# Kernel optimization log

Hardware: AMD Instinct MI355X
Metric: run time of the kernel (lower is better)

The kernel has to match this reference:

```python
import jax, jax.numpy as jnp
import numpy as np

HEADS = 8
HEIGHT = 512
WIDTH = 512
LATENT = 64  # height // 8
N_INST = 8


def setup_inputs() -> dict:
    key = jax.random.key(0)
    ks = jax.random.split(key, 8)
    C, Cx, L, N = 320, 768, 77, N_INST
    HW = LATENT * LATENT
    hidden_states = jax.random.normal(ks[0], (2, HW, C), jnp.float32)
    encoder_hidden_states = jax.random.normal(ks[1], (N + 3, L, Cx), jnp.float32)
    # non-degenerate normalized boxes (x0, y0, x1, y1)
    rng = np.random.default_rng(0)
    x0 = rng.uniform(0.0, 0.5, (N,)).astype(np.float32)
    y0 = rng.uniform(0.0, 0.5, (N,)).astype(np.float32)
    x1 = (x0 + rng.uniform(0.2, 0.45, (N,))).astype(np.float32)
    y1 = (y0 + rng.uniform(0.2, 0.45, (N,))).astype(np.float32)
    bboxes = jnp.asarray(np.stack([x0, y0, x1, y1], axis=-1)[None], jnp.float32)  # (1, N, 4)
    s = 0.02
    Wq = jax.random.normal(ks[2], (C, C), jnp.float32) * s
    Wk = jax.random.normal(ks[3], (Cx, C), jnp.float32) * s
    Wv = jax.random.normal(ks[4], (Cx, C), jnp.float32) * s
    Wo = jax.random.normal(ks[5], (C, C), jnp.float32) * s
    bo = jnp.zeros((C,), jnp.float32)
    return dict(hidden_states=hidden_states, encoder_hidden_states=encoder_hidden_states,
                bboxes=bboxes, Wq=Wq, Wk=Wk, Wv=Wv, Wo=Wo, bo=bo)


def _heads(x):
    # (B, S, H*D) -> (B*H, S, D)   [diffusers head_to_batch_dim]
    B, S, C = x.shape
    D = C // HEADS
    return x.reshape(B, S, HEADS, D).transpose(0, 2, 1, 3).reshape(B * HEADS, S, D)


def _unheads(x):
    # (B*H, S, D) -> (B, S, H*D)   [diffusers batch_to_head_dim]
    BH, S, D = x.shape
    B = BH // HEADS
    return x.reshape(B, HEADS, S, D).transpose(0, 2, 1, 3).reshape(B, S, HEADS * D)


def _forward(hidden_states, encoder_hidden_states, bboxes, Wq, Wk, Wv, Wo, bo):
    N = bboxes.shape[1]
    HW = hidden_states.shape[1]
    # drop the extra (MIGC) text embedding row, as in the processor
    ehs = encoder_hidden_states[:-1]  # (N+2, L, Cx)
    # batch = [uncond, cond repeated instance_num+1 times]
    hs = jnp.concatenate([hidden_states[:1],
                          jnp.repeat(hidden_states[1:2], N + 1, axis=0)], axis=0)  # (N+2, HW, C)
    q = _heads(hs @ Wq)
    k = _heads(ehs @ Wk)
    v = _heads(ehs @ Wv)
    scale = 1.0 / jnp.sqrt(jnp.asarray(q.shape[-1], q.dtype))
    probs = jax.nn.softmax(jnp.einsum('bqd,bkd->bqk', q, k) * scale, axis=-1)  # ((N+2)*H, HW, L)
    out = _unheads(jnp.einsum('bqk,bkd->bqd', probs, v))  # (N+2, HW, C)
    out = out @ Wo + bo
    hs_uncond = out[:1]
    cond_ca = out[1:][None]  # (1, N+1, HW, C)
    # rasterize per-instance bbox masks at full res (int() truncation == floor for positives)
    b = bboxes[0]  # (N, 4) = x0, y0, x1, y1
    w_min = jnp.floor(WIDTH * b[:, 0])[:, None, None]
    w_max = jnp.floor(WIDTH * b[:, 2])[:, None, None]
    h_min = jnp.floor(HEIGHT * b[:, 1])[:, None, None]
    h_max = jnp.floor(HEIGHT * b[:, 3])[:, None, None]
    rows = jnp.arange(HEIGHT, dtype=jnp.float32)[None, :, None]
    cols = jnp.arange(WIDTH, dtype=jnp.float32)[None, None, :]
    masks = ((rows >= h_min) & (rows < h_max) & (cols >= w_min) & (cols < w_max)).astype(jnp.float32)  # (N,H,W)
    gmask = jax.image.resize(masks, (N, LATENT, LATENT), method='bilinear')  # (N, 64, 64)
    # NaiveFuser: phase weights = [0.1 (full prompt), 10*mask_i], normalized sum over phases
    phase_w = jnp.concatenate([jnp.full((1, HW), 0.1, jnp.float32),
                               gmask.reshape(N, HW) * 10.0], axis=0)  # (N+1, HW)
    w = phase_w[None, :, :, None]  # (1, N+1, HW, 1)
    fused = (cond_ca * w).sum(axis=1) / (w.sum(axis=1) + 1e-6)  # (1, HW, C)
    return jnp.concatenate([hs_uncond, fused], axis=0)  # (2, HW, C)


def reference(hidden_states, encoder_hidden_states, bboxes, Wq, Wk, Wv, Wo, bo):
    return _forward(hidden_states, encoder_hidden_states, bboxes, Wq, Wk, Wv, Wo, bo)
```

## Files before the change

kernel.cpp:

```cpp
#include <hip/hip_runtime.h>
#include <math.h>

#define HW 4096
#define C 320
#define CX 768
#define L 77
#define NB 10
#define NH 8
#define HD 40
#define NINST 8
#define KVC 640
#define SCALE 0.15811388300841898f
#define PSTR 104
#define KSTR 48
#define VSTR 104

typedef _Float16 half8v __attribute__((ext_vector_type(8)));
typedef _Float16 half4v __attribute__((ext_vector_type(4)));
typedef float f32x4 __attribute__((ext_vector_type(4)));

#define KBH (80 * KSTR)
#define VBH (48 * VSTR)

#define SEG_MASK   16
#define N_CVT1     (2 * HW * C / 4)
#define N_CVT2     (NB * L * CX / 4)
#define SEG_CVT    (((N_CVT1 + N_CVT2) + 255) / 256)
#define SEG_WPACK  240
#define SEG_VTZ    195
#define SEG_KPAD   6
#define NPREP      (SEG_MASK + SEG_CVT + SEG_WPACK + SEG_VTZ + SEG_KPAD)

__device__ __forceinline__ float axis_profile(int o, float lo, float hi) {
    float num = 0.f, den = 0.f;
    int j0 = 8 * o - 4;
#pragma unroll
    for (int t = 0; t < 16; ++t) {
        int j = j0 + t;
        float wt = 1.0f - fabsf((float)t - 7.5f) * 0.125f;
        if (j >= 0 && j < 512) {
            den += wt;
            float fj = (float)j;
            if (fj >= lo && fj < hi) num += wt;
        }
    }
    return num / den;
}

__global__ __launch_bounds__(256) void prep_kernel(
        const float* __restrict__ bboxes,
        const float* __restrict__ hs, const float* __restrict__ ehs,
        const float* __restrict__ Wq, const float* __restrict__ Wk,
        const float* __restrict__ Wv, const float* __restrict__ Wo,
        float* __restrict__ wPh, float* __restrict__ wSum,
        _Float16* __restrict__ hsH, _Float16* __restrict__ ehsH,
        _Float16* __restrict__ WqT, _Float16* __restrict__ WkvT,
        _Float16* __restrict__ WoT, _Float16* __restrict__ VTg,
        _Float16* __restrict__ Khp) {
    __shared__ float tile[64][65];
    __shared__ float sw_s[NINST][64];
    __shared__ float sh_s[NINST][4];
    int bx = blockIdx.x, tid = threadIdx.x;

    if (bx < SEG_MASK) {
        int oyb = bx * 4;
        for (int i = tid; i < NINST * 64; i += 256) {
            int n = i >> 6, ox = i & 63;
            float lo = floorf(512.f * bboxes[n * 4 + 0]);
            float hi = floorf(512.f * bboxes[n * 4 + 2]);
            sw_s[n][ox] = axis_profile(ox, lo, hi);
        }
        if (tid < NINST * 4) {
            int n = tid >> 2, oy = tid & 3;
            float lo = floorf(512.f * bboxes[n * 4 + 1]);
            float hi = floorf(512.f * bboxes[n * 4 + 3]);
            sh_s[n][oy] = axis_profile(oyb + oy, lo, hi);
        }
        __syncthreads();
        int oy = tid >> 6, ox = tid & 63;
        int hw = (oyb + oy) * 64 + ox;
        float sum = 0.1f;
        wPh[hw] = 0.1f;
#pragma unroll
        for (int n = 0; n < NINST; ++n) {
            float wv = 10.f * sh_s[n][oy] * sw_s[n][ox];
            wPh[(n + 1) * HW + hw] = wv;
            sum += wv;
        }
        wSum[hw] = sum;
    } else if (bx < SEG_MASK + SEG_CVT) {
        int i = (bx - SEG_MASK) * 256 + tid;
        const float* src; _Float16* dst;
        if (i < N_CVT1) { src = hs; dst = hsH; }
        else if (i < N_CVT1 + N_CVT2) { i -= N_CVT1; src = ehs; dst = ehsH; }
        else return;
        float4 v = ((const float4*)src)[i];
        half4v h = {(_Float16)v.x, (_Float16)v.y, (_Float16)v.z, (_Float16)v.w};
        ((half4v*)dst)[i] = h;
    } else if (bx < SEG_MASK + SEG_CVT + SEG_WPACK) {
        int zz = bx - SEG_MASK - SEG_CVT;
        int z = zz / 60, inner = zz - z * 60;
        int by = inner / 5, bx2 = inner - by * 5;
        const float* W; _Float16* WT; int K;
        if (z == 0)      { W = Wq; WT = WqT; K = C; }
        else if (z == 1) { W = Wk; WT = WkvT; K = CX; }
        else if (z == 2) { W = Wv; WT = WkvT + (size_t)C * CX; K = CX; }
        else             { W = Wo; WT = WoT; K = C; }
        int kt = by * 64;
        if (kt >= K) return;
        int nt = bx2 * 64;
#pragma unroll
        for (int p = 0; p < 16; ++p) {
            int idx = p * 256 + tid;
            int k = idx >> 6, n = idx & 63;
            tile[k][n] = W[(size_t)(kt + k) * C + nt + n];
        }
        __syncthreads();
#pragma unroll
        for (int p = 0; p < 16; ++p) {
            int idx = p * 256 + tid;
            int n = idx >> 6, k = idx & 63;
            WT[(size_t)(nt + n) * K + kt + k] = (_Float16)tile[k][n];
        }
    } else if (bx < SEG_MASK + SEG_CVT + SEG_WPACK + SEG_VTZ) {
        int i = (bx - SEG_MASK - SEG_CVT - SEG_WPACK) * 256 + tid;
        int e0 = i * 8;
        int rem = e0 % VBH;
        int d = rem / VSTR;
        int key0 = rem % VSTR;
        half8v v;
#pragma unroll
        for (int j = 0; j < 8; ++j)
            v[j] = (_Float16)((d == 40 && (key0 + j) < 77) ? 1.f : 0.f);
        ((half8v*)VTg)[i] = v;
    } else {
        int i = (bx - SEG_MASK - SEG_CVT - SEG_WPACK - SEG_VTZ) * 256 + tid;
        if (i < 1440) {
            int rowIdx = i / 6, c8 = i - rowIdx * 6;
            int bh = rowIdx / 3;
            int key = 77 + rowIdx - bh * 3;
            half8v z8 = {(_Float16)0.f,(_Float16)0.f,(_Float16)0.f,(_Float16)0.f,
                         (_Float16)0.f,(_Float16)0.f,(_Float16)0.f,(_Float16)0.f};
            *(half8v*)(Khp + ((size_t)bh * 80 + key) * KSTR + c8 * 8) = z8;
        }
    }
}

__global__ __launch_bounds__(256) void gemm_kv(const _Float16* __restrict__ A,
                                               const _Float16* __restrict__ BT,
                                               _Float16* __restrict__ Khp,
                                               _Float16* __restrict__ VTg) {
    const int K = CX, M = NB * L;
    int lane = threadIdx.x & 63, wave = threadIdx.x >> 6;
    int m0 = blockIdx.y * 64 + wave * 16;
    int n0 = blockIdx.x * 64;
    int lr = lane & 15, kq = (lane >> 4) * 8;
    int arow = m0 + lr; if (arow >= M) arow = M - 1;
    const _Float16* ap = A + (size_t)arow * K + kq;
    const _Float16* bp = BT + (size_t)(n0 + lr) * K + kq;
    f32x4 acc0 = {0.f,0.f,0.f,0.f}, acc1 = acc0, acc2 = acc0, acc3 = acc0;
    for (int k0 = 0; k0 < K; k0 += 32) {
        half8v af = *(const half8v*)(ap + k0);
        half8v b0 = *(const half8v*)(bp + k0);
        half8v b1 = *(const half8v*)(bp + (size_t)16 * K + k0);
        half8v b2 = *(const half8v*)(bp + (size_t)32 * K + k0);
        half8v b3 = *(const half8v*)(bp + (size_t)48 * K + k0);
        acc0 = __builtin_amdgcn_mfma_f32_16x16x32_f16(af, b0, acc0, 0, 0, 0);
        acc1 = __builtin_amdgcn_mfma_f32_16x16x32_f16(af, b1, acc1, 0, 0, 0);
        acc2 = __builtin_amdgcn_mfma_f32_16x16x32_f16(af, b2, acc2, 0, 0, 0);
        acc3 = __builtin_amdgcn_mfma_f32_16x16x32_f16(af, b3, acc3, 0, 0, 0);
    }
    int rb = m0 + ((lane >> 4) << 2);
    f32x4 accs[4] = {acc0, acc1, acc2, acc3};
#pragma unroll
    for (int t = 0; t < 4; ++t) {
        int col = n0 + t * 16 + lr;
#pragma unroll
        for (int r = 0; r < 4; ++r) {
            int row = rb + r;
            if (row < M) {
                int bb = row / 77;
                int key = row - bb * 77;
                if (col < C) {
                    int h = col / HD, d = col - h * HD;
                    Khp[((size_t)(bb * 8 + h) * 80 + key) * KSTR + d] = (_Float16)accs[t][r];
                } else {
                    int ch = col - C;
                    int h = ch / HD, d = ch - h * HD;
                    VTg[((size_t)(bb * 8 + h) * 48 + d) * VSTR + key] = (_Float16)accs[t][r];
                }
            }
        }
    }
}

__global__ __launch_bounds__(256, 2) void attn_mfma(const _Float16* __restrict__ hsH,
                                                    const _Float16* __restrict__ WqT,
                                                    const _Float16* __restrict__ Khp,
                                                    const _Float16* __restrict__ VTg,
                                                    const float* __restrict__ wPh,
                                                    _Float16* __restrict__ Xh) {
    __shared__ _Float16 smem[2 * (KBH + VBH) + 4 * 2 * 16 * PSTR];
    _Float16* Ks0 = smem;
    _Float16* Vs0 = smem + KBH;
    _Float16* Ks1 = smem + KBH + VBH;
    _Float16* Vs1 = smem + 2 * KBH + VBH;
    _Float16* pbase = smem + 2 * (KBH + VBH);

    int tid = threadIdx.x;
    int wave = tid >> 6, lane = tid & 63;
    int head = blockIdx.x >> 6;
    int qg = blockIdx.x & 63;
    int qrow0 = qg * 64 + wave * 16;
    int c = lane & 15, quad = lane >> 4;
    _Float16* pl0 = pbase + (size_t)(wave * 2) * 16 * PSTR;
    _Float16* pl1 = pl0 + 16 * PSTR;
    half8v zero8 = {(_Float16)0.f,(_Float16)0.f,(_Float16)0.f,(_Float16)0.f,
                    (_Float16)0.f,(_Float16)0.f,(_Float16)0.f,(_Float16)0.f};

    const half8v* Kg8 = (const half8v*)(Khp + (size_t)head * KBH);
    const half8v* Vg8 = (const half8v*)(VTg + (size_t)head * VBH);
    const size_t kstep = (size_t)8 * KBH / 8;
    const size_t vstep = (size_t)8 * VBH / 8;

    half8v kr0, kr1, vr0, vr1, vr2;
    kr0 = Kg8[tid];
    if (tid < 224) kr1 = Kg8[tid + 256];
    vr0 = Vg8[tid];
    vr1 = Vg8[tid + 256];
    if (tid < 112) vr2 = Vg8[tid + 512];

#pragma unroll
    for (int i = 0; i < 4; ++i) {
        int idx = i * 64 + lane;
        if (idx < 224) {
            int buf = idx / 112;
            int rem = idx - buf * 112;
            int row = rem / 7, ch = rem - row * 7;
            _Float16* pb = buf ? pl1 : pl0;
            *(half8v*)&pb[row * PSTR + 40 + ch * 8] = zero8;
        }
    }

    {
        const _Float16* bu = hsH + (size_t)(qrow0 + c) * C + quad * 8;
        const _Float16* bc = bu + (size_t)HW * C;
        f32x4 qa0[3] = {}, qa1[3] = {};
        for (int k0 = 0; k0 < C; k0 += 32) {
            half8v hu = *(const half8v*)(bu + k0);
            half8v hc = *(const half8v*)(bc + k0);
#pragma unroll
            for (int t = 0; t < 3; ++t) {
                const _Float16* ap = WqT + (size_t)(head * HD + t * 16 + c) * C + quad * 8 + k0;
                half8v af = *(const half8v*)ap;
                qa0[t] = __builtin_amdgcn_mfma_f32_16x16x32_f16(af, hu, qa0[t], 0, 0, 0);
                qa1[t] = __builtin_amdgcn_mfma_f32_16x16x32_f16(af, hc, qa1[t], 0, 0, 0);
            }
        }
#pragma unroll
        for (int t = 0; t < 3; ++t) {
            if (t < 2 || quad < 2) {
                half4v h0 = {(_Float16)(qa0[t][0] * SCALE), (_Float16)(qa0[t][1] * SCALE),
                             (_Float16)(qa0[t][2] * SCALE), (_Float16)(qa0[t][3] * SCALE)};
                half4v h1 = {(_Float16)(qa1[t][0] * SCALE), (_Float16)(qa1[t][1] * SCALE),
                             (_Float16)(qa1[t][2] * SCALE), (_Float16)(qa1[t][3] * SCALE)};
                *(half4v*)(pl0 + c * PSTR + t * 16 + quad * 4) = h0;
                *(half4v*)(pl1 + c * PSTR + t * 16 + quad * 4) = h1;
            }
        }
    }
    half8v qu0 = *(const half8v*)(pl0 + (size_t)c * PSTR + quad * 8);
    half8v qu1 = *(const half8v*)(pl0 + (size_t)c * PSTR + 32 + quad * 8);
    half8v qc0 = *(const half8v*)(pl1 + (size_t)c * PSTR + quad * 8);
    half8v qc1 = *(const half8v*)(pl1 + (size_t)c * PSTR + 32 + quad * 8);

    {
        half8v* Kd = (half8v*)Ks0;
        half8v* Vd = (half8v*)Vs0;
        Kd[tid] = kr0;
        if (tid < 224) Kd[tid + 256] = kr1;
        Vd[tid] = vr0;
        Vd[tid + 256] = vr1;
        if (tid < 112) Vd[tid + 512] = vr2;
    }
    __syncthreads();

    f32x4 oacc[3] = {};
    int srcl = 32 + c;

    for (int b = 0; b < NB; ++b) {
        if (b + 1 < NB) {
            const half8v* Kn = Kg8 + (size_t)(b + 1) * 8 * (KBH / 8);
            const half8v* Vn = Vg8 + (size_t)(b + 1) * 8 * (VBH / 8);
            kr0 = Kn[tid];
            if (tid < 224) kr1 = Kn[tid + 256];
            vr0 = Vn[tid];
            vr1 = Vn[tid + 256];
            if (tid < 112) vr2 = Vn[tid + 512];
        }

        _Float16* Kb = (b & 1) ? Ks1 : Ks0;
        _Float16* Vb = (b & 1) ? Vs1 : Vs0;
        half8v qb0 = b ? qc0 : qu0;
        half8v qb1 = b ? qc1 : qu1;
        float w = b ? wPh[(size_t)(b - 1) * HW + qrow0 + c] : 1.f;

        f32x4 s[5];
#pragma unroll
        for (int u = 0; u < 5; ++u) {
            half8v ka0 = *(const half8v*)&Kb[(u * 16 + c) * KSTR + quad * 8];
            half8v ka1 = *(const half8v*)&Kb[(u * 16 + c) * KSTR + 32 + quad * 8];
            f32x4 a = {0.f,0.f,0.f,0.f};
            a = __builtin_amdgcn_mfma_f32_16x16x32_f16(ka0, qb0, a, 0, 0, 0);
            a = __builtin_amdgcn_mfma_f32_16x16x32_f16(ka1, qb1, a, 0, 0, 0);
            s[u] = a;
        }

#pragma unroll
        for (int u = 0; u < 5; ++u) {
            half4v h = {(_Float16)__expf(s[u][0]), (_Float16)__expf(s[u][1]),
                        (_Float16)__expf(s[u][2]), (_Float16)__expf(s[u][3])};
            *(half4v*)(pl0 + c * PSTR + u * 16 + quad * 4) = h;
        }
        half8v p0 = *(const half8v*)(pl0 + (size_t)c * PSTR + quad * 8);
        half8v p1 = *(const half8v*)(pl0 + (size_t)c * PSTR + 32 + quad * 8);
        half8v p2 = *(const half8v*)(pl0 + (size_t)c * PSTR + 64 + quad * 8);

        f32x4 ox[3];
#pragma unroll
        for (int t = 0; t < 3; ++t) {
            half8v va0 = *(const half8v*)&Vb[(t * 16 + c) * VSTR + quad * 8];
            half8v va1 = *(const half8v*)&Vb[(t * 16 + c) * VSTR + 32 + quad * 8];
            half8v va2 = *(const half8v*)&Vb[(t * 16 + c) * VSTR + 64 + quad * 8];
            f32x4 a = {0.f,0.f,0.f,0.f};
            a = __builtin_amdgcn_mfma_f32_16x16x32_f16(va0, p0, a, 0, 0, 0);
            a = __builtin_amdgcn_mfma_f32_16x16x32_f16(va1, p1, a, 0, 0, 0);
            a = __builtin_amdgcn_mfma_f32_16x16x32_f16(va2, p2, a, 0, 0, 0);
            ox[t] = a;
        }

        float l = __shfl(ox[2][0], srcl, 64);

        if (b == 0) {
            float rin = 1.0f / l;
#pragma unroll
            for (int t = 0; t < 3; ++t) {
                if (t < 2 || quad < 2) {
                    half4v h = {(_Float16)(ox[t][0] * rin), (_Float16)(ox[t][1] * rin),
                                (_Float16)(ox[t][2] * rin), (_Float16)(ox[t][3] * rin)};
                    *(half4v*)(Xh + (size_t)(qrow0 + c) * C + head * HD + t * 16 + quad * 4) = h;
                }
            }
        } else {
            float rf = w / l;
#pragma unroll
            for (int t = 0; t < 3; ++t) {
                oacc[t][0] += ox[t][0] * rf;
                oacc[t][1] += ox[t][1] * rf;
                oacc[t][2] += ox[t][2] * rf;
                oacc[t][3] += ox[t][3] * rf;
            }
        }

        if (b + 1 < NB) {
            half8v* Kd = (half8v*)((b & 1) ? Ks0 : Ks1);
            half8v* Vd = (half8v*)((b & 1) ? Vs0 : Vs1);
            Kd[tid] = kr0;
            if (tid < 224) Kd[tid + 256] = kr1;
            Vd[tid] = vr0;
            Vd[tid + 256] = vr1;
            if (tid < 112) Vd[tid + 512] = vr2;
        }
        __syncthreads();
    }

#pragma unroll
    for (int t = 0; t < 3; ++t) {
        if (t < 2 || quad < 2) {
            half4v h = {(_Float16)oacc[t][0], (_Float16)oacc[t][1],
                        (_Float16)oacc[t][2], (_Float16)oacc[t][3]};
            *(half4v*)(Xh + (size_t)(HW + qrow0 + c) * C + head * HD + t * 16 + quad * 4) = h;
        }
    }
}

__global__ __launch_bounds__(256) void gemm_oproj_f16(const _Float16* __restrict__ A,
                                                      const _Float16* __restrict__ BT,
                                                      const float* __restrict__ bo,
                                                      const float* __restrict__ wSum,
                                                      float* __restrict__ Out) {
    const int K = C;
    __shared__ _Float16 Bs[64 * 328];
    int tid = threadIdx.x;
    int n0 = blockIdx.x * 64;
    for (int i = tid; i < 64 * 40; i += 256) {
        int row = i / 40, c8 = i - row * 40;
        *(half8v*)&Bs[row * 328 + c8 * 8] =
            *(const half8v*)(BT + (size_t)(n0 + row) * K + c8 * 8);
    }
    __syncthreads();

    int lane = tid & 63, wave = tid >> 6;
    int m0 = blockIdx.y * 64 + wave * 16;
    int lr = lane & 15, kq = (lane >> 4) * 8;
    const _Float16* ap = A + (size_t)(m0 + lr) * K + kq;
    f32x4 acc0 = {0.f,0.f,0.f,0.f}, acc1 = acc0, acc2 = acc0, acc3 = acc0;
#pragma unroll
    for (int k0 = 0; k0 < K; k0 += 32) {
        half8v af = *(const half8v*)(ap + k0);
        half8v b0 = *(const half8v*)&Bs[(0 * 16 + lr) * 328 + k0 + kq];
        half8v b1 = *(const half8v*)&Bs[(1 * 16 + lr) * 328 + k0 + kq];
        half8v b2 = *(const half8v*)&Bs[(2 * 16 + lr) * 328 + k0 + kq];
        half8v b3 = *(const half8v*)&Bs[(3 * 16 + lr) * 328 + k0 + kq];
        acc0 = __builtin_amdgcn_mfma_f32_16x16x32_f16(af, b0, acc0, 0, 0, 0);
        acc1 = __builtin_amdgcn_mfma_f32_16x16x32_f16(af, b1, acc1, 0, 0, 0);
        acc2 = __builtin_amdgcn_mfma_f32_16x16x32_f16(af, b2, acc2, 0, 0, 0);
        acc3 = __builtin_amdgcn_mfma_f32_16x16x32_f16(af, b3, acc3, 0, 0, 0);
    }
    int rb = m0 + ((lane >> 4) << 2);
    f32x4 accs[4] = {acc0, acc1, acc2, acc3};
#pragma unroll
    for (int t = 0; t < 4; ++t) {
        int col = n0 + t * 16 + lr;
        float bv = bo[col];
#pragma unroll
        for (int r = 0; r < 4; ++r) {
            int row = rb + r;
            float v = accs[t][r];
            if (row < HW) {
                v += bv;
            } else {
                float ws = wSum[row - HW];
                v = (v + bv * ws) / (ws + 1e-6f);
            }
            Out[(size_t)row * C + col] = v;
        }
    }
}

extern "C" void kernel_launch(void* const* d_in, const int* in_sizes, int n_in,
                              void* d_out, int out_size, void* d_ws, size_t ws_size,
                              hipStream_t stream) {
    const float* hs   = (const float*)d_in[0];
    const float* ehs  = (const float*)d_in[1];
    const float* bbox = (const float*)d_in[2];
    const float* Wq   = (const float*)d_in[3];
    const float* Wk   = (const float*)d_in[4];
    const float* Wv   = (const float*)d_in[5];
    const float* Wo   = (const float*)d_in[6];
    const float* bo   = (const float*)d_in[7];
    float* out = (float*)d_out;

    float* wPh  = (float*)d_ws;
    float* wSum = wPh + (size_t)9 * HW;
    _Float16* hsH  = (_Float16*)(wSum + HW);
    _Float16* ehsH = hsH + (size_t)2 * HW * C;
    _Float16* WqT  = ehsH + (size_t)NB * L * CX;
    _Float16* WkvT = WqT + (size_t)C * C;
    _Float16* WoT  = WkvT + (size_t)KVC * CX;
    _Float16* Khp  = WoT + (size_t)C * C;
    _Float16* VTg  = Khp + (size_t)80 * KBH;
    _Float16* Xh   = VTg + (size_t)80 * VBH;

    prep_kernel<<<dim3(NPREP), 256, 0, stream>>>(bbox, hs, ehs, Wq, Wk, Wv, Wo,
                                                 wPh, wSum, hsH, ehsH, WqT, WkvT, WoT,
                                                 VTg, Khp);
    gemm_kv<<<dim3(KVC / 64, (NB * L + 63) / 64), 256, 0, stream>>>(ehsH, WkvT, Khp, VTg);
    attn_mfma<<<dim3(NH * 64), 256, 0, stream>>>(hsH, WqT, Khp, VTg, wPh, Xh);
    gemm_oproj_f16<<<dim3(C / 64, (2 * HW) / 64), 256, 0, stream>>>(Xh, WoT, bo, wSum, out);
}
```

Baseline: 132.8 us.

## Fuse four kernel launches into one cooperative persistent kernel with grid syncs

Replaces the prep, KV-GEMM, attention and output-projection launches with a single cooperative kernel that loops over work units per stage and separates stages with grid.sync(). The goal is to remove three kernel-launch gaps and their tail effects. In exchange, the grid is capped at 512 blocks (or the occupancy limit), and some stages such as prep (over 600 units) and oproj (640 units) must loop. Grid-wide barriers also add their own cost. A fallback to the original four launches is kept in case the cooperative launch fails.

Result: slower. 264.6 us (+99.3%).

```diff
diff --git a/kernel.cpp b/kernel.cpp
--- a/kernel.cpp
+++ b/kernel.cpp
@@ -1,5 +1,8 @@
 #include <hip/hip_runtime.h>
+#include <hip/hip_cooperative_groups.h>
 #include <math.h>
+
+namespace cg = cooperative_groups;
 
 #define HW 4096
 #define C 320
@@ -31,6 +34,11 @@
 #define SEG_KPAD   6
 #define NPREP      (SEG_MASK + SEG_CVT + SEG_WPACK + SEG_VTZ + SEG_KPAD)
 
+#define KV_UNITS    130
+#define ATTN_UNITS  (NH * 64)
+#define OPROJ_UNITS 640
+#define SMEM_BYTES  61952
+
 __device__ __forceinline__ float axis_profile(int o, float lo, float hi) {
     float num = 0.f, den = 0.f;
     int j0 = 8 * o - 4;
@@ -45,6 +53,398 @@
         }
     }
     return num / den;
+}
+
+__global__ __launch_bounds__(256, 2) void fused_kernel(
+        const float* __restrict__ bboxes, const float* __restrict__ hs,
+        const float* __restrict__ ehs, const float* __restrict__ Wq,
+        const float* __restrict__ Wk, const float* __restrict__ Wv,
+        const float* __restrict__ Wo, const float* __restrict__ bo,
+        float* __restrict__ wPh, float* __restrict__ wSum,
+        _Float16* __restrict__ hsH, _Float16* __restrict__ ehsH,
+        _Float16* __restrict__ WqT, _Float16* __restrict__ WkvT,
+        _Float16* __restrict__ WoT, _Float16* __restrict__ Khp,
+        _Float16* __restrict__ VTg, _Float16* __restrict__ Xh,
+        float* __restrict__ Out) {
+    cg::grid_group grid = cg::this_grid();
+    __shared__ __align__(16) unsigned char smem_raw[SMEM_BYTES];
+    const int tid = threadIdx.x;
+    const int gsz = gridDim.x;
+
+    {
+        float (*tile)[65] = (float (*)[65])smem_raw;
+        float (*sw_s)[64] = (float (*)[64])(smem_raw + 64 * 65 * 4);
+        float (*sh_s)[4]  = (float (*)[4])(smem_raw + 64 * 65 * 4 + NINST * 64 * 4);
+        for (int s = blockIdx.x; s < NPREP; s += gsz) {
+            if (s < SEG_MASK) {
+                int oyb = s * 4;
+                for (int i = tid; i < NINST * 64; i += 256) {
+                    int n = i >> 6, ox = i & 63;
+                    float lo = floorf(512.f * bboxes[n * 4 + 0]);
+                    float hi = floorf(512.f * bboxes[n * 4 + 2]);
+                    sw_s[n][ox] = axis_profile(ox, lo, hi);
+                }
+                if (tid < NINST * 4) {
+                    int n = tid >> 2, oy = tid & 3;
+                    float lo = floorf(512.f * bboxes[n * 4 + 1]);
+                    float hi = floorf(512.f * bboxes[n * 4 + 3]);
+                    sh_s[n][oy] = axis_profile(oyb + oy, lo, hi);
+                }
+                __syncthreads();
+                int oy = tid >> 6, ox = tid & 63;
+                int hw = (oyb + oy) * 64 + ox;
+                float sum = 0.1f;
+                wPh[hw] = 0.1f;
+#pragma unroll
+                for (int n = 0; n < NINST; ++n) {
+                    float wv = 10.f * sh_s[n][oy] * sw_s[n][ox];
+                    wPh[(n + 1) * HW + hw] = wv;
+                    sum += wv;
+                }
+                wSum[hw] = sum;
+            } else if (s < SEG_MASK + SEG_CVT) {
+                int i = (s - SEG_MASK) * 256 + tid;
+                if (i < N_CVT1) {
+                    float4 v = ((const float4*)hs)[i];
+                    half4v h = {(_Float16)v.x, (_Float16)v.y, (_Float16)v.z, (_Float16)v.w};
+                    ((half4v*)hsH)[i] = h;
+                } else if (i < N_CVT1 + N_CVT2) {
+                    int j = i - N_CVT1;
+                    float4 v = ((const float4*)ehs)[j];
+                    half4v h = {(_Float16)v.x, (_Float16)v.y, (_Float16)v.z, (_Float16)v.w};
+                    ((half4v*)ehsH)[j] = h;
+                }
+            } else if (s < SEG_MASK + SEG_CVT + SEG_WPACK) {
+                int zz = s - SEG_MASK - SEG_CVT;
+                int z = zz / 60, inner = zz - z * 60;
+                int by = inner / 5, bx2 = inner - by * 5;
+                const float* W; _Float16* WT; int K;
+                if (z == 0)      { W = Wq; WT = WqT; K = C; }
+                else if (z == 1) { W = Wk; WT = WkvT; K = CX; }
+                else if (z == 2) { W = Wv; WT = WkvT + (size_t)C * CX; K = CX; }
+                else             { W = Wo; WT = WoT; K = C; }
+                int kt = by * 64;
+                if (kt < K) {
+                    int nt = bx2 * 64;
+#pragma unroll
+                    for (int p = 0; p < 16; ++p) {
+                        int idx = p * 256 + tid;
+                        int k = idx >> 6, n = idx & 63;
+                        tile[k][n] = W[(size_t)(kt + k) * C + nt + n];
+                    }
+                    __syncthreads();
+#pragma unroll
+                    for (int p = 0; p < 16; ++p) {
+                        int idx = p * 256 + tid;
+                        int n = idx >> 6, k = idx & 63;
+                        WT[(size_t)(nt + n) * K + kt + k] = (_Float16)tile[k][n];
+                    }
+                }
+            } else if (s < SEG_MASK + SEG_CVT + SEG_WPACK + SEG_VTZ) {
+                int i = (s - SEG_MASK - SEG_CVT - SEG_WPACK) * 256 + tid;
+                int e0 = i * 8;
+                int rem = e0 % VBH;
+                int d = rem / VSTR;
+                int key0 = rem % VSTR;
+                half8v v;
+#pragma unroll
+                for (int j = 0; j < 8; ++j)
+                    v[j] = (_Float16)((d == 40 && (key0 + j) < 77) ? 1.f : 0.f);
+                ((half8v*)VTg)[i] = v;
+            } else {
+                int i = (s - SEG_MASK - SEG_CVT - SEG_WPACK - SEG_VTZ) * 256 + tid;
+                if (i < 1440) {
+                    int rowIdx = i / 6, c8 = i - rowIdx * 6;
+                    int bh = rowIdx / 3;
+                    int key = 77 + rowIdx - bh * 3;
+                    half8v z8 = {(_Float16)0.f,(_Float16)0.f,(_Float16)0.f,(_Float16)0.f,
+                                 (_Float16)0.f,(_Float16)0.f,(_Float16)0.f,(_Float16)0.f};
+                    *(half8v*)(Khp + ((size_t)bh * 80 + key) * KSTR + c8 * 8) = z8;
+                }
+            }
+            __syncthreads();
+        }
+    }
+    grid.sync();
+
+    for (int u = blockIdx.x; u < KV_UNITS; u += gsz) {
+        const int K = CX, M = NB * L;
+        int lane = tid & 63, wave = tid >> 6;
+        int m0 = (u / 10) * 64 + wave * 16;
+        int n0 = (u % 10) * 64;
+        int lr = lane & 15, kq = (lane >> 4) * 8;
+        int arow = m0 + lr; if (arow >= M) arow = M - 1;
+        const _Float16* ap = ehsH + (size_t)arow * K + kq;
+        const _Float16* bp = WkvT + (size_t)(n0 + lr) * K + kq;
+        f32x4 acc0 = {0.f,0.f,0.f,0.f}, acc1 = acc0, acc2 = acc0, acc3 = acc0;
+        for (int k0 = 0; k0 < K; k0 += 32) {
+            half8v af = *(const half8v*)(ap + k0);
+            half8v b0 = *(const half8v*)(bp + k0);
+            half8v b1 = *(const half8v*)(bp + (size_t)16 * K + k0);
+            half8v b2 = *(const half8v*)(bp + (size_t)32 * K + k0);
+            half8v b3 = *(const half8v*)(bp + (size_t)48 * K + k0);
+            acc0 = __builtin_amdgcn_mfma_f32_16x16x32_f16(af, b0, acc0, 0, 0, 0);
+            acc1 = __builtin_amdgcn_mfma_f32_16x16x32_f16(af, b1, acc1, 0, 0, 0);
+            acc2 = __builtin_amdgcn_mfma_f32_16x16x32_f16(af, b2, acc2, 0, 0, 0);
+            acc3 = __builtin_amdgcn_mfma_f32_16x16x32_f16(af, b3, acc3, 0, 0, 0);
+        }
+        int rb = m0 + ((lane >> 4) << 2);
+        f32x4 accs[4] = {acc0, acc1, acc2, acc3};
+#pragma unroll
+        for (int t = 0; t < 4; ++t) {
+            int col = n0 + t * 16 + lr;
+#pragma unroll
+            for (int r = 0; r < 4; ++r) {
+                int row = rb + r;
+                if (row < M) {
+                    int bb = row / 77;
+                    int key = row - bb * 77;
+                    if (col < C) {
+                        int h = col / HD, d = col - h * HD;
+                        Khp[((size_t)(bb * 8 + h) * 80 + key) * KSTR + d] = (_Float16)accs[t][r];
+                    } else {
+                        int ch = col - C;
+                        int h = ch / HD, d = ch - h * HD;
+                        VTg[((size_t)(bb * 8 + h) * 48 + d) * VSTR + key] = (_Float16)accs[t][r];
+                    }
+                }
+            }
+        }
+    }
+    grid.sync();
+
+    for (int u = blockIdx.x; u < ATTN_UNITS; u += gsz) {
+        _Float16* smemH = (_Float16*)smem_raw;
+        _Float16* Ks0 = smemH;
+        _Float16* Vs0 = smemH + KBH;
+        _Float16* Ks1 = smemH + KBH + VBH;
+        _Float16* Vs1 = smemH + 2 * KBH + VBH;
+        _Float16* pbase = smemH + 2 * (KBH + VBH);
+
+        int wave = tid >> 6, lane = tid & 63;
+        int head = u >> 6;
+        int qg = u & 63;
+        int qrow0 = qg * 64 + wave * 16;
+        int c = lane & 15, quad = lane >> 4;
+        _Float16* pl0 = pbase + (size_t)(wave * 2) * 16 * PSTR;
+        _Float16* pl1 = pl0 + 16 * PSTR;
+        half8v zero8 = {(_Float16)0.f,(_Float16)0.f,(_Float16)0.f,(_Float16)0.f,
+                        (_Float16)0.f,(_Float16)0.f,(_Float16)0.f,(_Float16)0.f};
+
+        const half8v* Kg8 = (const half8v*)(Khp + (size_t)head * KBH);
+        const half8v* Vg8 = (const half8v*)(VTg + (size_t)head * VBH);
+
+        half8v kr0, kr1, vr0, vr1, vr2;
+        kr0 = Kg8[tid];
+        if (tid < 224) kr1 = Kg8[tid + 256];
+        vr0 = Vg8[tid];
+        vr1 = Vg8[tid + 256];
+        if (tid < 112) vr2 = Vg8[tid + 512];
+
+#pragma unroll
+        for (int i = 0; i < 4; ++i) {
+            int idx = i * 64 + lane;
+            if (idx < 224) {
+                int buf = idx / 112;
+                int rem = idx - buf * 112;
+                int row = rem / 7, ch = rem - row * 7;
+                _Float16* pb = buf ? pl1 : pl0;
+                *(half8v*)&pb[row * PSTR + 40 + ch * 8] = zero8;
+            }
+        }
+
+        {
+            const _Float16* bu = hsH + (size_t)(qrow0 + c) * C + quad * 8;
+            const _Float16* bc = bu + (size_t)HW * C;
+            f32x4 qa0[3] = {}, qa1[3] = {};
+            for (int k0 = 0; k0 < C; k0 += 32) {
+                half8v hu = *(const half8v*)(bu + k0);
+                half8v hc = *(const half8v*)(bc + k0);
+#pragma unroll
+                for (int t = 0; t < 3; ++t) {
+                    const _Float16* ap = WqT + (size_t)(head * HD + t * 16 + c) * C + quad * 8 + k0;
+                    half8v af = *(const half8v*)ap;
+                    qa0[t] = __builtin_amdgcn_mfma_f32_16x16x32_f16(af, hu, qa0[t], 0, 0, 0);
+                    qa1[t] = __builtin_amdgcn_mfma_f32_16x16x32_f16(af, hc, qa1[t], 0, 0, 0);
+                }
+            }
+#pragma unroll
+            for (int t = 0; t < 3; ++t) {
+                if (t < 2 || quad < 2) {
+                    half4v h0 = {(_Float16)(qa0[t][0] * SCALE), (_Float16)(qa0[t][1] * SCALE),
+                                 (_Float16)(qa0[t][2] * SCALE), (_Float16)(qa0[t][3] * SCALE)};
+                    half4v h1 = {(_Float16)(qa1[t][0] * SCALE), (_Float16)(qa1[t][1] * SCALE),
+                                 (_Float16)(qa1[t][2] * SCALE), (_Float16)(qa1[t][3] * SCALE)};
+                    *(half4v*)(pl0 + c * PSTR + t * 16 + quad * 4) = h0;
+                    *(half4v*)(pl1 + c * PSTR + t * 16 + quad * 4) = h1;
+                }
+            }
+        }
+        half8v qu0 = *(const half8v*)(pl0 + (size_t)c * PSTR + quad * 8);
+        half8v qu1 = *(const half8v*)(pl0 + (size_t)c * PSTR + 32 + quad * 8);
+        half8v qc0 = *(const half8v*)(pl1 + (size_t)c * PSTR + quad * 8);
+        half8v qc1 = *(const half8v*)(pl1 + (size_t)c * PSTR + 32 + quad * 8);
+
+        {
+            half8v* Kd = (half8v*)Ks0;
+            half8v* Vd = (half8v*)Vs0;
+            Kd[tid] = kr0;
+            if (tid < 224) Kd[tid + 256] = kr1;
+            Vd[tid] = vr0;
+            Vd[tid + 256] = vr1;
+            if (tid < 112) Vd[tid + 512] = vr2;
+        }
+        __syncthreads();
+
+        f32x4 oacc[3] = {};
+        int srcl = 32 + c;
+
+        for (int b = 0; b < NB; ++b) {
+            if (b + 1 < NB) {
+                const half8v* Kn = Kg8 + (size_t)(b + 1) * 8 * (KBH / 8);
+                const half8v* Vn = Vg8 + (size_t)(b + 1) * 8 * (VBH / 8);
+                kr0 = Kn[tid];
+                if (tid < 224) kr1 = Kn[tid + 256];
+                vr0 = Vn[tid];
+                vr1 = Vn[tid + 256];
+                if (tid < 112) vr2 = Vn[tid + 512];
+            }
+
+            _Float16* Kb = (b & 1) ? Ks1 : Ks0;
+            _Float16* Vb = (b & 1) ? Vs1 : Vs0;
+            half8v qb0 = b ? qc0 : qu0;
+            half8v qb1 = b ? qc1 : qu1;
+            float w = b ? wPh[(size_t)(b - 1) * HW + qrow0 + c] : 1.f;
+
+            f32x4 s[5];
+#pragma unroll
+            for (int v = 0; v < 5; ++v) {
+                half8v ka0 = *(const half8v*)&Kb[(v * 16 + c) * KSTR + quad * 8];
+                half8v ka1 = *(const half8v*)&Kb[(v * 16 + c) * KSTR + 32 + quad * 8];
+                f32x4 a = {0.f,0.f,0.f,0.f};
+                a = __builtin_amdgcn_mfma_f32_16x16x32_f16(ka0, qb0, a, 0, 0, 0);
+                a = __builtin_amdgcn_mfma_f32_16x16x32_f16(ka1, qb1, a, 0, 0, 0);
+                s[v] = a;
+            }
+
+#pragma unroll
+            for (int v = 0; v < 5; ++v) {
+                half4v h = {(_Float16)__expf(s[v][0]), (_Float16)__expf(s[v][1]),
+                            (_Float16)__expf(s[v][2]), (_Float16)__expf(s[v][3])};
+                *(half4v*)(pl0 + c * PSTR + v * 16 + quad * 4) = h;
+            }
+            half8v p0 = *(const half8v*)(pl0 + (size_t)c * PSTR + quad * 8);
+            half8v p1 = *(const half8v*)(pl0 + (size_t)c * PSTR + 32 + quad * 8);
+            half8v p2 = *(const half8v*)(pl0 + (size_t)c * PSTR + 64 + quad * 8);
+
+            f32x4 ox[3];
+#pragma unroll
+            for (int t = 0; t < 3; ++t) {
+                half8v va0 = *(const half8v*)&Vb[(t * 16 + c) * VSTR + quad * 8];
+                half8v va1 = *(const half8v*)&Vb[(t * 16 + c) * VSTR + 32 + quad * 8];
+                half8v va2 = *(const half8v*)&Vb[(t * 16 + c) * VSTR + 64 + quad * 8];
+                f32x4 a = {0.f,0.f,0.f,0.f};
+                a = __builtin_amdgcn_mfma_f32_16x16x32_f16(va0, p0, a, 0, 0, 0);
+                a = __builtin_amdgcn_mfma_f32_16x16x32_f16(va1, p1, a, 0, 0, 0);
+                a = __builtin_amdgcn_mfma_f32_16x16x32_f16(va2, p2, a, 0, 0, 0);
+                ox[t] = a;
+            }
+
+            float l = __shfl(ox[2][0], srcl, 64);
+
+            if (b == 0) {
+                float rin = 1.0f / l;
+#pragma unroll
+                for (int t = 0; t < 3; ++t) {
+                    if (t < 2 || quad < 2) {
+                        half4v h = {(_Float16)(ox[t][0] * rin), (_Float16)(ox[t][1] * rin),
+                                    (_Float16)(ox[t][2] * rin), (_Float16)(ox[t][3] * rin)};
+                        *(half4v*)(Xh + (size_t)(qrow0 + c) * C + head * HD + t * 16 + quad * 4) = h;
+                    }
+                }
+            } else {
+                float rf = w / l;
+#pragma unroll
+                for (int t = 0; t < 3; ++t) {
+                    oacc[t][0] += ox[t][0] * rf;
+                    oacc[t][1] += ox[t][1] * rf;
+                    oacc[t][2] += ox[t][2] * rf;
+                    oacc[t][3] += ox[t][3] * rf;
+                }
+            }
+
+            if (b + 1 < NB) {
+                half8v* Kd = (half8v*)((b & 1) ? Ks0 : Ks1);
+                half8v* Vd = (half8v*)((b & 1) ? Vs0 : Vs1);
+                Kd[tid] = kr0;
+                if (tid < 224) Kd[tid + 256] = kr1;
+                Vd[tid] = vr0;
+                Vd[tid + 256] = vr1;
+                if (tid < 112) Vd[tid + 512] = vr2;
+            }
+            __syncthreads();
+        }
+
+#pragma unroll
+        for (int t = 0; t < 3; ++t) {
+            if (t < 2 || quad < 2) {
+                half4v h = {(_Float16)oacc[t][0], (_Float16)oacc[t][1],
+                            (_Float16)oacc[t][2], (_Float16)oacc[t][3]};
+                *(half4v*)(Xh + (size_t)(HW + qrow0 + c) * C + head * HD + t * 16 + quad * 4) = h;
+            }
+        }
+    }
+    grid.sync();
+
+    for (int u = blockIdx.x; u < OPROJ_UNITS; u += gsz) {
+        _Float16* Bs = (_Float16*)smem_raw;
+        const int K = C;
+        int n0 = (u % 5) * 64;
+        for (int i = tid; i < 64 * 40; i += 256) {
+            int row = i / 40, c8 = i - row * 40;
+            *(half8v*)&Bs[row * 328 + c8 * 8] =
+                *(const half8v*)(WoT + (size_t)(n0 + row) * K + c8 * 8);
+        }
+        __syncthreads();
+
+        int lane = tid & 63, wave = tid >> 6;
+        int m0 = (u / 5) * 64 + wave * 16;
+        int lr = lane & 15, kq = (lane >> 4) * 8;
+        const _Float16* ap = Xh + (size_t)(m0 + lr) * K + kq;
+        f32x4 acc0 = {0.f,0.f,0.f,0.f}, acc1 = acc0, acc2 = acc0, acc3 = acc0;
+#pragma unroll
+        for (int k0 = 0; k0 < K; k0 += 32) {
+            half8v af = *(const half8v*)(ap + k0);
+            half8v b0 = *(const half8v*)&Bs[(0 * 16 + lr) * 328 + k0 + kq];
+            half8v b1 = *(const half8v*)&Bs[(1 * 16 + lr) * 328 + k0 + kq];
+            half8v b2 = *(const half8v*)&Bs[(2 * 16 + lr) * 328 + k0 + kq];
+            half8v b3 = *(const half8v*)&Bs[(3 * 16 + lr) * 328 + k0 + kq];
+            acc0 = __builtin_amdgcn_mfma_f32_16x16x32_f16(af, b0, acc0, 0, 0, 0);
+            acc1 = __builtin_amdgcn_mfma_f32_16x16x32_f16(af, b1, acc1, 0, 0, 0);
+            acc2 = __builtin_amdgcn_mfma_f32_16x16x32_f16(af, b2, acc2, 0, 0, 0);
+            acc3 = __builtin_amdgcn_mfma_f32_16x16x32_f16(af, b3, acc3, 0, 0, 0);
+        }
+        int rb = m0 + ((lane >> 4) << 2);
+        f32x4 accs[4] = {acc0, acc1, acc2, acc3};
+#pragma unroll
+        for (int t = 0; t < 4; ++t) {
+            int col = n0 + t * 16 + lr;
+            float bv = bo[col];
+#pragma unroll
+            for (int r = 0; r < 4; ++r) {
+                int row = rb + r;
+                float v = accs[t][r];
+                if (row < HW) {
+                    v += bv;
+                } else {
+                    float ws = wSum[row - HW];
+                    v = (v + bv * ws) / (ws + 1e-6f);
+                }
+                Out[(size_t)row * C + col] = v;
+            }
+        }
+        __syncthreads();
+    }
 }
 
 __global__ __launch_bounds__(256) void prep_kernel(
@@ -220,8 +620,6 @@
 
     const half8v* Kg8 = (const half8v*)(Khp + (size_t)head * KBH);
     const half8v* Vg8 = (const half8v*)(VTg + (size_t)head * VBH);
-    const size_t kstep = (size_t)8 * KBH / 8;
-    const size_t vstep = (size_t)8 * VBH / 8;
 
     half8v kr0, kr1, vr0, vr1, vr2;
     kr0 = Kg8[tid];
@@ -462,10 +860,44 @@
     _Float16* VTg  = Khp + (size_t)80 * KBH;
     _Float16* Xh   = VTg + (size_t)80 * VBH;
 
-    prep_kernel<<<dim3(NPREP), 256, 0, stream>>>(bbox, hs, ehs, Wq, Wk, Wv, Wo,
-                                                 wPh, wSum, hsH, ehsH, WqT, WkvT, WoT,
-                                                 VTg, Khp);
-    gemm_kv<<<dim3(KVC / 64, (NB * L + 63) / 64), 256, 0, stream>>>(ehsH, WkvT, Khp, VTg);
-    attn_mfma<<<dim3(NH * 64), 256, 0, stream>>>(hsH, WqT, Khp, VTg, wPh, Xh);
-    gemm_oproj_f16<<<dim3(C / 64, (2 * HW) / 64), 256, 0, stream>>>(Xh, WoT, bo, wSum, out);
+    static int nblk = -1;
+    if (nblk < 0) {
+        int dev = 0;
+        (void)hipGetDevice(&dev);
+        int coop = 0;
+        (void)hipDeviceGetAttribute(&coop, hipDeviceAttributeCooperativeLaunch, dev);
+        if (!coop) {
+            nblk = 0;
+        } else {
+            int per_cu = 0;
+            if (hipOccupancyMaxActiveBlocksPerMultiprocessor(
+                    &per_cu, (const void*)fused_kernel, 256, 0) != hipSuccess || per_cu <= 0)
+                per_cu = 2;
+            int ncu = 256;
+            hipDeviceProp_t prop;
+            if (hipGetDeviceProperties(&prop, dev) == hipSuccess && prop.multiProcessorCount > 0)
+                ncu = prop.multiProcessorCount;
+            long cap = (long)per_cu * (long)ncu;
+            nblk = cap < ATTN_UNITS ? (int)cap : ATTN_UNITS;
+            if (nblk < 1) nblk = 1;
+        }
+    }
+
+    hipError_t err = hipErrorUnknown;
+    if (nblk > 0) {
+        void* args[] = {(void*)&bbox, (void*)&hs, (void*)&ehs, (void*)&Wq, (void*)&Wk,
+                        (void*)&Wv, (void*)&Wo, (void*)&bo, (void*)&wPh, (void*)&wSum,
+                        (void*)&hsH, (void*)&ehsH, (void*)&WqT, (void*)&WkvT, (void*)&WoT,
+                        (void*)&Khp, (void*)&VTg, (void*)&Xh, (void*)&out};
+        err = hipLaunchCooperativeKernel((const void*)fused_kernel, dim3(nblk), dim3(256),
+                                         args, 0, stream);
+    }
+    if (err != hipSuccess) {
+        prep_kernel<<<dim3(NPREP), 256, 0, stream>>>(bbox, hs, ehs, Wq, Wk, Wv, Wo,
+                                                     wPh, wSum, hsH, ehsH, WqT, WkvT, WoT,
+                                                     VTg, Khp);
+        gemm_kv<<<dim3(KVC / 64, (NB * L + 63) / 64), 256, 0, stream>>>(ehsH, WkvT, Khp, VTg);
+        attn_mfma<<<dim3(NH * 64), 256, 0, stream>>>(hsH, WqT, Khp, VTg, wPh, Xh);
+        gemm_oproj_f16<<<dim3(C / 64, (2 * HW) / 64), 256, 0, stream>>>(Xh, WoT, bo, wSum, out);
+    }
 }
```

## Fuse K/V projection GEMM into prep kernel reading fp32 inputs directly

Applied to the files above, without the earlier changes.

The separate gemm_kv launch is folded into the prep kernel as an extra block segment. That segment converts fp32 encoder states and Wk/Wv to fp16 on the fly, so the ehs conversion pass and the Wk/Wv transpose-pack pass are no longer needed. The V padding init is narrowed to write only the pad regions (rows 40-47 and keys 77-103), so it no longer overwrites the whole buffer and races with the fused GEMM writes. This drops one launch and several intermediate buffers. The cost is strided scalar fp32 weight loads in the GEMM inner loop, which are much less coalesced than the old packed fp16 loads.

Result: no change. 133.0 us (+0.1%).

```diff
diff --git a/kernel.cpp b/kernel.cpp
--- a/kernel.cpp
+++ b/kernel.cpp
@@ -22,14 +22,15 @@
 #define KBH (80 * KSTR)
 #define VBH (48 * VSTR)
 
+#define SEG_KV     130
 #define SEG_MASK   16
 #define N_CVT1     (2 * HW * C / 4)
-#define N_CVT2     (NB * L * CX / 4)
-#define SEG_CVT    (((N_CVT1 + N_CVT2) + 255) / 256)
-#define SEG_WPACK  240
-#define SEG_VTZ    195
+#define SEG_CVTH   (N_CVT1 / 256)
+#define SEG_WPK    50
+#define SEG_VT40   33
+#define SEG_VTP    338
 #define SEG_KPAD   6
-#define NPREP      (SEG_MASK + SEG_CVT + SEG_WPACK + SEG_VTZ + SEG_KPAD)
+#define NPREP (SEG_KV + SEG_MASK + SEG_CVTH + SEG_WPK + SEG_VT40 + SEG_VTP + SEG_KPAD)
 
 __device__ __forceinline__ float axis_profile(int o, float lo, float hi) {
     float num = 0.f, den = 0.f;
@@ -47,23 +48,80 @@
     return num / den;
 }
 
-__global__ __launch_bounds__(256) void prep_kernel(
+__global__ __launch_bounds__(256) void prep_kv_kernel(
         const float* __restrict__ bboxes,
         const float* __restrict__ hs, const float* __restrict__ ehs,
         const float* __restrict__ Wq, const float* __restrict__ Wk,
         const float* __restrict__ Wv, const float* __restrict__ Wo,
         float* __restrict__ wPh, float* __restrict__ wSum,
-        _Float16* __restrict__ hsH, _Float16* __restrict__ ehsH,
-        _Float16* __restrict__ WqT, _Float16* __restrict__ WkvT,
-        _Float16* __restrict__ WoT, _Float16* __restrict__ VTg,
-        _Float16* __restrict__ Khp) {
+        _Float16* __restrict__ hsH,
+        _Float16* __restrict__ WqT, _Float16* __restrict__ WoT,
+        _Float16* __restrict__ VTg, _Float16* __restrict__ Khp) {
     __shared__ float tile[64][65];
     __shared__ float sw_s[NINST][64];
     __shared__ float sh_s[NINST][4];
     int bx = blockIdx.x, tid = threadIdx.x;
 
-    if (bx < SEG_MASK) {
-        int oyb = bx * 4;
+    if (bx < SEG_KV) {
+        const int K = CX, M = NB * L;
+        int lane = tid & 63, wave = tid >> 6;
+        int m0 = (bx / 10) * 64 + wave * 16;
+        int n0 = (bx % 10) * 64;
+        int lr = lane & 15, kq = (lane >> 4) * 8;
+        int arow = m0 + lr; if (arow >= M) arow = M - 1;
+        const float* ap = ehs + (size_t)arow * K + kq;
+        const float* wp[4];
+        int cols[4];
+#pragma unroll
+        for (int t = 0; t < 4; ++t) {
+            int col = n0 + t * 16 + lr;
+            cols[t] = col;
+            wp[t] = (col < C) ? (Wk + col) : (Wv + (col - C));
+        }
+        f32x4 acc0 = {0.f,0.f,0.f,0.f}, acc1 = acc0, acc2 = acc0, acc3 = acc0;
+        for (int k0 = 0; k0 < K; k0 += 32) {
+            float4 a0 = *(const float4*)(ap + k0);
+            float4 a1 = *(const float4*)(ap + k0 + 4);
+            half8v af = {(_Float16)a0.x, (_Float16)a0.y, (_Float16)a0.z, (_Float16)a0.w,
+                         (_Float16)a1.x, (_Float16)a1.y, (_Float16)a1.z, (_Float16)a1.w};
+            half8v bf0, bf1, bf2, bf3;
+#pragma unroll
+            for (int j = 0; j < 8; ++j) {
+                size_t kk = (size_t)(k0 + kq + j) * C;
+                bf0[j] = (_Float16)wp[0][kk];
+                bf1[j] = (_Float16)wp[1][kk];
+                bf2[j] = (_Float16)wp[2][kk];
+                bf3[j] = (_Float16)wp[3][kk];
+            }
+            acc0 = __builtin_amdgcn_mfma_f32_16x16x32_f16(af, bf0, acc0, 0, 0, 0);
+            acc1 = __builtin_amdgcn_mfma_f32_16x16x32_f16(af, bf1, acc1, 0, 0, 0);
+            acc2 = __builtin_amdgcn_mfma_f32_16x16x32_f16(af, bf2, acc2, 0, 0, 0);
+            acc3 = __builtin_amdgcn_mfma_f32_16x16x32_f16(af, bf3, acc3, 0, 0, 0);
+        }
+        int rb = m0 + ((lane >> 4) << 2);
+        f32x4 accs[4] = {acc0, acc1, acc2, acc3};
+#pragma unroll
+        for (int t = 0; t < 4; ++t) {
+            int col = cols[t];
+#pragma unroll
+            for (int r = 0; r < 4; ++r) {
+                int row = rb + r;
+                if (row < M) {
+                    int bb = row / 77;
+                    int key = row - bb * 77;
+                    if (col < C) {
+                        int h = col / HD, d = col - h * HD;
+                        Khp[((size_t)(bb * 8 + h) * 80 + key) * KSTR + d] = (_Float16)accs[t][r];
+                    } else {
+                        int ch = col - C;
+                        int h = ch / HD, d = ch - h * HD;
+                        VTg[((size_t)(bb * 8 + h) * 48 + d) * VSTR + key] = (_Float16)accs[t][r];
+                    }
+                }
+            }
+        }
+    } else if (bx < SEG_KV + SEG_MASK) {
+        int oyb = (bx - SEG_KV) * 4;
         for (int i = tid; i < NINST * 64; i += 256) {
             int n = i >> 6, ox = i & 63;
             float lo = floorf(512.f * bboxes[n * 4 + 0]);
@@ -88,27 +146,18 @@
             sum += wv;
         }
         wSum[hw] = sum;
-    } else if (bx < SEG_MASK + SEG_CVT) {
-        int i = (bx - SEG_MASK) * 256 + tid;
-        const float* src; _Float16* dst;
-        if (i < N_CVT1) { src = hs; dst = hsH; }
-        else if (i < N_CVT1 + N_CVT2) { i -= N_CVT1; src = ehs; dst = ehsH; }
-        else return;
-        float4 v = ((const float4*)src)[i];
+    } else if (bx < SEG_KV + SEG_MASK + SEG_CVTH) {
+        int i = (bx - SEG_KV - SEG_MASK) * 256 + tid;
+        float4 v = ((const float4*)hs)[i];
         half4v h = {(_Float16)v.x, (_Float16)v.y, (_Float16)v.z, (_Float16)v.w};
-        ((half4v*)dst)[i] = h;
-    } else if (bx < SEG_MASK + SEG_CVT + SEG_WPACK) {
-        int zz = bx - SEG_MASK - SEG_CVT;
-        int z = zz / 60, inner = zz - z * 60;
+        ((half4v*)hsH)[i] = h;
+    } else if (bx < SEG_KV + SEG_MASK + SEG_CVTH + SEG_WPK) {
+        int zz = bx - SEG_KV - SEG_MASK - SEG_CVTH;
+        int z = zz / 25, inner = zz - z * 25;
         int by = inner / 5, bx2 = inner - by * 5;
-        const float* W; _Float16* WT; int K;
-        if (z == 0)      { W = Wq; WT = WqT; K = C; }
-        else if (z == 1) { W = Wk; WT = WkvT; K = CX; }
-        else if (z == 2) { W = Wv; WT = WkvT + (size_t)C * CX; K = CX; }
-        else             { W = Wo; WT = WoT; K = C; }
-        int kt = by * 64;
-        if (kt >= K) return;
-        int nt = bx2 * 64;
+        const float* W = z ? Wo : Wq;
+        _Float16* WT = z ? WoT : WqT;
+        int kt = by * 64, nt = bx2 * 64;
 #pragma unroll
         for (int p = 0; p < 16; ++p) {
             int idx = p * 256 + tid;
@@ -120,21 +169,29 @@
         for (int p = 0; p < 16; ++p) {
             int idx = p * 256 + tid;
             int n = idx >> 6, k = idx & 63;
-            WT[(size_t)(nt + n) * K + kt + k] = (_Float16)tile[k][n];
-        }
-    } else if (bx < SEG_MASK + SEG_CVT + SEG_WPACK + SEG_VTZ) {
-        int i = (bx - SEG_MASK - SEG_CVT - SEG_WPACK) * 256 + tid;
-        int e0 = i * 8;
-        int rem = e0 % VBH;
-        int d = rem / VSTR;
-        int key0 = rem % VSTR;
-        half8v v;
-#pragma unroll
-        for (int j = 0; j < 8; ++j)
-            v[j] = (_Float16)((d == 40 && (key0 + j) < 77) ? 1.f : 0.f);
-        ((half8v*)VTg)[i] = v;
+            WT[(size_t)(nt + n) * C + kt + k] = (_Float16)tile[k][n];
+        }
+    } else if (bx < SEG_KV + SEG_MASK + SEG_CVTH + SEG_WPK + SEG_VT40) {
+        int i = (bx - SEG_KV - SEG_MASK - SEG_CVTH - SEG_WPK) * 256 + tid;
+        if (i < 8320) {
+            int bh = i / 104, rem = i - bh * 104;
+            int d = 40 + rem / 13, c8 = rem - (rem / 13) * 13;
+            int key0 = c8 * 8;
+            half8v v;
+#pragma unroll
+            for (int j = 0; j < 8; ++j)
+                v[j] = (_Float16)((d == 40 && (key0 + j) < 77) ? 1.f : 0.f);
+            *(half8v*)(VTg + (size_t)bh * VBH + (size_t)d * VSTR + key0) = v;
+        }
+    } else if (bx < SEG_KV + SEG_MASK + SEG_CVTH + SEG_WPK + SEG_VT40 + SEG_VTP) {
+        int i = (bx - SEG_KV - SEG_MASK - SEG_CVTH - SEG_WPK - SEG_VT40) * 256 + tid;
+        if (i < 86400) {
+            int r = i / 27, kk = 77 + (i - r * 27);
+            int bh = r / 40, d = r - bh * 40;
+            VTg[(size_t)bh * VBH + (size_t)d * VSTR + kk] = (_Float16)0.f;
+        }
     } else {
-        int i = (bx - SEG_MASK - SEG_CVT - SEG_WPACK - SEG_VTZ) * 256 + tid;
+        int i = (bx - SEG_KV - SEG_MASK - SEG_CVTH - SEG_WPK - SEG_VT40 - SEG_VTP) * 256 + tid;
         if (i < 1440) {
             int rowIdx = i / 6, c8 = i - rowIdx * 6;
             int bh = rowIdx / 3;
@@ -142,54 +199,6 @@
             half8v z8 = {(_Float16)0.f,(_Float16)0.f,(_Float16)0.f,(_Float16)0.f,
                          (_Float16)0.f,(_Float16)0.f,(_Float16)0.f,(_Float16)0.f};
             *(half8v*)(Khp + ((size_t)bh * 80 + key) * KSTR + c8 * 8) = z8;
-        }
-    }
-}
-
-__global__ __launch_bounds__(256) void gemm_kv(const _Float16* __restrict__ A,
-                                               const _Float16* __restrict__ BT,
-                                               _Float16* __restrict__ Khp,
-                                               _Float16* __restrict__ VTg) {
-    const int K = CX, M = NB * L;
-    int lane = threadIdx.x & 63, wave = threadIdx.x >> 6;
-    int m0 = blockIdx.y * 64 + wave * 16;
-    int n0 = blockIdx.x * 64;
-    int lr = lane & 15, kq = (lane >> 4) * 8;
-    int arow = m0 + lr; if (arow >= M) arow = M - 1;
-    const _Float16* ap = A + (size_t)arow * K + kq;
-    const _Float16* bp = BT + (size_t)(n0 + lr) * K + kq;
-    f32x4 acc0 = {0.f,0.f,0.f,0.f}, acc1 = acc0, acc2 = acc0, acc3 = acc0;
-    for (int k0 = 0; k0 < K; k0 += 32) {
-        half8v af = *(const half8v*)(ap + k0);
-        half8v b0 = *(const half8v*)(bp + k0);
-        half8v b1 = *(const half8v*)(bp + (size_t)16 * K + k0);
-        half8v b2 = *(const half8v*)(bp + (size_t)32 * K + k0);
-        half8v b3 = *(const half8v*)(bp + (size_t)48 * K + k0);
-        acc0 = __builtin_amdgcn_mfma_f32_16x16x32_f16(af, b0, acc0, 0, 0, 0);
-        acc1 = __builtin_amdgcn_mfma_f32_16x16x32_f16(af, b1, acc1, 0, 0, 0);
-        acc2 = __builtin_amdgcn_mfma_f32_16x16x32_f16(af, b2, acc2, 0, 0, 0);
-        acc3 = __builtin_amdgcn_mfma_f32_16x16x32_f16(af, b3, acc3, 0, 0, 0);
-    }
-    int rb = m0 + ((lane >> 4) << 2);
-    f32x4 accs[4] = {acc0, acc1, acc2, acc3};
-#pragma unroll
-    for (int t = 0; t < 4; ++t) {
-        int col = n0 + t * 16 + lr;
-#pragma unroll
-        for (int r = 0; r < 4; ++r) {
-            int row = rb + r;
-            if (row < M) {
-                int bb = row / 77;
-                int key = row - bb * 77;
-                if (col < C) {
-                    int h = col / HD, d = col - h * HD;
-                    Khp[((size_t)(bb * 8 + h) * 80 + key) * KSTR + d] = (_Float16)accs[t][r];
-                } else {
-                    int ch = col - C;
-                    int h = ch / HD, d = ch - h * HD;
-                    VTg[((size_t)(bb * 8 + h) * 48 + d) * VSTR + key] = (_Float16)accs[t][r];
-                }
-            }
         }
     }
 }
@@ -220,8 +229,6 @@
 
     const half8v* Kg8 = (const half8v*)(Khp + (size_t)head * KBH);
     const half8v* Vg8 = (const half8v*)(VTg + (size_t)head * VBH);
-    const size_t kstep = (size_t)8 * KBH / 8;
-    const size_t vstep = (size_t)8 * VBH / 8;
 
     half8v kr0, kr1, vr0, vr1, vr2;
     kr0 = Kg8[tid];
@@ -462,10 +469,8 @@
     _Float16* VTg  = Khp + (size_t)80 * KBH;
     _Float16* Xh   = VTg + (size_t)80 * VBH;
 
-    prep_kernel<<<dim3(NPREP), 256, 0, stream>>>(bbox, hs, ehs, Wq, Wk, Wv, Wo,
-                                                 wPh, wSum, hsH, ehsH, WqT, WkvT, WoT,
-                                                 VTg, Khp);
-    gemm_kv<<<dim3(KVC / 64, (NB * L + 63) / 64), 256, 0, stream>>>(ehsH, WkvT, Khp, VTg);
+    prep_kv_kernel<<<dim3(NPREP), 256, 0, stream>>>(bbox, hs, ehs, Wq, Wk, Wv, Wo,
+                                                    wPh, wSum, hsH, WqT, WoT, VTg, Khp);
     attn_mfma<<<dim3(NH * 64), 256, 0, stream>>>(hsH, WqT, Khp, VTg, wPh, Xh);
     gemm_oproj_f16<<<dim3(C / 64, (2 * HW) / 64), 256, 0, stream>>>(Xh, WoT, bo, wSum, out);
 }
```
